# Kernel tuning notes

Measured on AMD Instinct MI355X. Metric: run time of the kernel, lower is better.

## Reference

```python
import jax, jax.numpy as jnp
import numpy as np

NUM_HEADS = 8
DIM = 256
SCALE = (DIM // NUM_HEADS) ** -0.5  # head_dim = dim // nhead = 32


def setup_inputs() -> dict:
    key = jax.random.key(0)
    k1, k2, k3, k4, k5 = jax.random.split(key, 5)
    B, N = 1, 4096
    qk = jax.random.normal(k1, (B, N, 3 * DIM), dtype=jnp.float32)
    v_cls = jax.random.normal(k2, (B, N, 2 * DIM), dtype=jnp.float32)
    masks = jax.random.uniform(k3, (B, N, N), dtype=jnp.float32)
    # torch Linear weights stored as [in, out] for x @ W
    W_qk = jax.random.normal(k4, (3 * DIM, 6 * DIM), dtype=jnp.float32) * (3 * DIM) ** -0.5
    W_v = jax.random.normal(k5, (2 * DIM, 2 * DIM), dtype=jnp.float32) * (2 * DIM) ** -0.5
    return {"qk": qk, "v_cls": v_cls, "masks": masks, "W_qk": W_qk, "W_v": W_v}


def reference(qk, v_cls, masks, W_qk, W_v):
    B, N, C_qk = qk.shape
    C_cls = v_cls.shape[-1]
    H = NUM_HEADS
    hd_qk = C_qk // H   # 96
    hd_v = C_cls // H   # 64

    # qk projection: [B,N,6*dim] -> (2,B,H,N,hd_qk)
    proj = (qk @ W_qk).reshape(B, N, 2, H, hd_qk).transpose(2, 0, 3, 1, 4)
    q, k = proj[0], proj[1]                      # [B,H,N,hd_qk]
    v = (v_cls @ W_v).reshape(B, N, H, hd_v).transpose(0, 2, 1, 3)  # [B,H,N,hd_v]

    attn = jnp.einsum('bhnd,bhmd->bhnm', q, k) * SCALE
    attn = jax.nn.softmax(attn, axis=-1)

    # post-softmax mask-mul and renorm by mask-sum and head count
    m = masks[:, None]                           # [B,1,N,N] broadcast over heads
    attn = attn * m / (H * jnp.sum(m, axis=-1, keepdims=True))
    # attn_drop with p=0.0 is identity in eval

    x_cls = jnp.einsum('bhnm,bhmd->bhnd', attn, v)
    return x_cls.transpose(0, 2, 1, 3).reshape(B, N, C_cls)
```

## Files before the change

### kernel.cpp

```cpp
#include <hip/hip_runtime.h>

typedef __attribute__((ext_vector_type(8))) _Float16 half8;
typedef __attribute__((ext_vector_type(4))) _Float16 half4;
typedef __attribute__((ext_vector_type(2))) _Float16 half2;
typedef __attribute__((ext_vector_type(2))) __fp16 fp16x2;
typedef __attribute__((ext_vector_type(4))) float f32x4;

#define N_SEQ 4096
#define HD_QK 96
#define HD_V  64
#define NHEADS 8
#define QSCALE 0.25505545556f
#define ESHIFT 8.0f

union PKC { fp16x2 p; half2 h; };

__device__ inline half2 pk_cvt(float a, float b) {
    PKC u;
    u.p = __builtin_amdgcn_cvt_pkrtz(a, b);
    return u.h;
}

__device__ inline half8 cvt8(float4 a, float4 b) {
    half8 h;
    h[0] = (_Float16)a.x; h[1] = (_Float16)a.y; h[2] = (_Float16)a.z; h[3] = (_Float16)a.w;
    h[4] = (_Float16)b.x; h[5] = (_Float16)b.y; h[6] = (_Float16)b.z; h[7] = (_Float16)b.w;
    return h;
}

__device__ inline void cast_blk(const float* __restrict__ in, _Float16* __restrict__ out,
                                int blk, int t) {
    size_t i = ((size_t)blk * 256 + t) * 8;
    float4 a = *(const float4*)(in + i);
    float4 b = *(const float4*)(in + i + 4);
    *(half8*)(out + i) = cvt8(a, b);
}

__global__ __launch_bounds__(256) void prep(
    const float* __restrict__ qk, const float* __restrict__ v_cls,
    const float* __restrict__ masks, const float* __restrict__ W_qk,
    const float* __restrict__ W_v,
    _Float16* __restrict__ Xh, _Float16* __restrict__ Vch,
    _Float16* __restrict__ Msw, float* __restrict__ Msum,
    _Float16* __restrict__ Wqkt, _Float16* __restrict__ Wvt)
{
    __shared__ float tile[32][33];
    const int bx = blockIdx.x, t = threadIdx.x;
    if (bx < 1536) {
        cast_blk(qk, Xh, bx, t);
    } else if (bx < 2560) {
        cast_blk(v_cls, Vch, bx - 1536, t);
    } else if (bx < 3968) {
        const bool big = bx < 3712;
        const int id = big ? bx - 2560 : bx - 3712;
        const int nx = big ? 48 : 16;
        const int C = big ? 1536 : 512, R = big ? 768 : 512;
        const float* in = big ? W_qk : W_v;
        _Float16* out = big ? Wqkt : Wvt;
        int cx = id % nx, cy = id / nx;
        int tx = t & 31, ty = t >> 5;
        int c0 = cx * 32, r0 = cy * 32;
        for (int k = 0; k < 4; k++)
            tile[ty + 8 * k][tx] = in[(size_t)(r0 + ty + 8 * k) * C + c0 + tx];
        __syncthreads();
        for (int k = 0; k < 4; k++)
            out[(size_t)(c0 + ty + 8 * k) * R + r0 + tx] = (_Float16)tile[tx][ty + 8 * k];
    } else {
        const int m = bx - 3968;
        const int q = m >> 1;
        const int k0 = (m & 1) * 2048 + t * 8;
        const float* src = masks + (size_t)q * N_SEQ + k0;
        float4 a = *(const float4*)src;
        float4 b = *(const float4*)(src + 4);
        const int q0b = q >> 6, l15 = q & 15, nt = (q >> 4) & 3;
        const int kb = k0 >> 6, wsl = (k0 >> 4) & 3, qd = (k0 >> 2) & 3;
        _Float16* dst = Msw + ((size_t)(q0b * 64 + kb) * 4 + wsl) * 1024
                            + l15 * 64 + qd * 16 + nt * 4;
        half4 h0 = {(_Float16)a.x, (_Float16)a.y, (_Float16)a.z, (_Float16)a.w};
        half4 h1 = {(_Float16)b.x, (_Float16)b.y, (_Float16)b.z, (_Float16)b.w};
        *(half4*)dst = h0;
        *(half4*)(dst + 16) = h1;
        float s = (a.x + a.y) + (a.z + a.w) + (b.x + b.y) + (b.z + b.w);
        for (int off = 1; off < 64; off <<= 1) s += __shfl_xor(s, off);
        if ((t & 63) == 0) atomicAdd(&Msum[q], s);
    }
}

__global__ __launch_bounds__(256) void proj_fused(
    const _Float16* __restrict__ Xh, const _Float16* __restrict__ Vch,
    const _Float16* __restrict__ Wqkt, const _Float16* __restrict__ Wvt,
    _Float16* __restrict__ Qh, _Float16* __restrict__ Kh,
    _Float16* __restrict__ Vtg)
{
    __shared__ _Float16 smem[2 * 128 * 72];
    _Float16 (*Xs)[72] = (_Float16 (*)[72])smem;
    _Float16 (*Ws)[72] = (_Float16 (*)[72])(smem + 128 * 72);

    const int t = threadIdx.x;
    const int lane = t & 63, wv = t >> 6;
    const int quad = lane >> 4, l15 = lane & 15;
    const bool qkmode = blockIdx.x < 12;
    const int n0 = qkmode ? blockIdx.x * 128 : (blockIdx.x - 12) * 128;
    const int row0 = blockIdx.y * 128;
    const int K = qkmode ? 768 : 512;
    const _Float16* X = qkmode ? Xh : Vch;
    const _Float16* Wt = qkmode ? Wqkt : Wvt;

    const int mB = (wv & 1) * 64, nB = (wv >> 1) * 64;
    const int sr = t >> 1, sk = (t & 1) * 32;

    const f32x4 fzero = {0.f, 0.f, 0.f, 0.f};
    f32x4 acc[4][4];
    for (int i = 0; i < 4; i++)
        for (int j = 0; j < 4; j++) acc[i][j] = fzero;

    for (int k0 = 0; k0 < K; k0 += 64) {
        __syncthreads();
        {
            const _Float16* xp = X + (size_t)(row0 + sr) * K + k0 + sk;
            *(half8*)&Xs[sr][sk]      = *(const half8*)xp;
            *(half8*)&Xs[sr][sk + 8]  = *(const half8*)(xp + 8);
            *(half8*)&Xs[sr][sk + 16] = *(const half8*)(xp + 16);
            *(half8*)&Xs[sr][sk + 24] = *(const half8*)(xp + 24);
            const _Float16* wp = Wt + (size_t)(n0 + sr) * K + k0 + sk;
            *(half8*)&Ws[sr][sk]      = *(const half8*)wp;
            *(half8*)&Ws[sr][sk + 8]  = *(const half8*)(wp + 8);
            *(half8*)&Ws[sr][sk + 16] = *(const half8*)(wp + 16);
            *(half8*)&Ws[sr][sk + 24] = *(const half8*)(wp + 24);
        }
        __syncthreads();
        for (int c = 0; c < 2; c++) {
            half8 af[4], bf[4];
            for (int i = 0; i < 4; i++)
                af[i] = *(const half8*)&Xs[mB + 16 * i + l15][c * 32 + quad * 8];
            for (int j = 0; j < 4; j++)
                bf[j] = *(const half8*)&Ws[nB + 16 * j + l15][c * 32 + quad * 8];
            for (int i = 0; i < 4; i++)
                for (int j = 0; j < 4; j++)
                    acc[i][j] = __builtin_amdgcn_mfma_f32_16x16x32_f16(af[i], bf[j], acc[i][j], 0, 0, 0);
        }
    }

    __syncthreads();
    _Float16 (*Ct)[136] = (_Float16 (*)[136])smem;
    for (int j = 0; j < 4; j++) {
        int col = n0 + nB + 16 * j + l15;
        float scl = (qkmode && col < 768) ? QSCALE : 1.0f;
        for (int i = 0; i < 4; i++)
            for (int r = 0; r < 4; r++)
                Ct[mB + 16 * i + quad * 4 + r][nB + 16 * j + l15] =
                    (_Float16)(acc[i][j][r] * scl);
    }
    __syncthreads();

    if (qkmode) {
        for (int e = 0; e < 8; e++) {
            int id = e * 256 + t;
            int row = id >> 4, cc = id & 15;
            int col = n0 + cc * 8;
            int w = col >= 768 ? 1 : 0;
            int rem = col - w * 768;
            int h = rem / 96, d = rem - h * 96;
            _Float16* dst = w ? Kh : Qh;
            *(half8*)&dst[((size_t)h * N_SEQ + row0 + row) * HD_QK + d] =
                *(const half8*)&Ct[row][cc * 8];
        }
    } else {
        for (int e = 0; e < 4; e++) {
            int id = e * 256 + t;
            int col = id >> 3, rc = id & 7;
            int c = n0 + col;
            int h = c >> 6, d = c & 63;
            half8 v0, v1;
            for (int k = 0; k < 8; k++) {
                v0[k] = Ct[rc * 16 + k][col];
                v1[k] = Ct[rc * 16 + 8 + k][col];
            }
            _Float16* dst = &Vtg[((size_t)h * HD_V + d) * N_SEQ + row0 + rc * 16];
            *(half8*)dst = v0;
            *(half8*)(dst + 8) = v1;
        }
    }
}

__global__ __launch_bounds__(256, 3) void flash_attn(
    const _Float16* __restrict__ Qh, const _Float16* __restrict__ Kh,
    const _Float16* __restrict__ Vtg, const _Float16* __restrict__ Msw,
    _Float16* __restrict__ Owsh, float* __restrict__ Lws)
{
    __shared__ __align__(16) float Ob[2][64][68];
    __shared__ float Lb[2][64];

    const int t = threadIdx.x;
    const int lane = t & 63, w = t >> 6;
    const int quad = lane >> 4, l15 = lane & 15;
    const int bx = blockIdx.x;
    const int q0b = bx & 63;
    const int hz = bx >> 6;
    const int head = hz & 7;
    const int z = hz >> 3;
    const int q0 = q0b * 64;
    const int kb0 = 21 * z, kbE = (z == 2) ? 64 : kb0 + 21;

    half8 qf[3][4];
    for (int nt = 0; nt < 4; nt++) {
        const _Float16* qp = Qh + ((size_t)head * N_SEQ + q0 + 16 * nt + l15) * HD_QK + 8 * quad;
        for (int c = 0; c < 3; c++)
            qf[c][nt] = *(const half8*)(qp + 32 * c);
    }

    const _Float16* kbase = Kh + ((size_t)head * N_SEQ + 16 * w + l15) * HD_QK + 8 * quad;
    const _Float16* vbase = Vtg + ((size_t)head * HD_V + l15) * N_SEQ + 16 * w + 4 * quad;
    const _Float16* mbase = Msw + ((size_t)(q0b * 64 + kb0) * 4 + w) * 1024
                                + (l15 * 4 + quad) * 16;

    const f32x4 fzero = {0.f, 0.f, 0.f, 0.f};
    f32x4 oacc[4][4];
    for (int nt = 0; nt < 4; nt++)
        for (int v = 0; v < 4; v++) oacc[nt][v] = fzero;
    float lsum[4] = {0.f, 0.f, 0.f, 0.f};

    half8 kf[3];
    half4 vf[4];
    half8 m01, m23;
    {
        const _Float16* kp = kbase + (size_t)kb0 * 64 * HD_QK;
        for (int c = 0; c < 3; c++) kf[c] = *(const half8*)(kp + 32 * c);
        const _Float16* vp = vbase + kb0 * 64;
        for (int v = 0; v < 4; v++) vf[v] = *(const half4*)(vp + (size_t)(16 * v) * N_SEQ);
        m01 = *(const half8*)mbase;
        m23 = *(const half8*)(mbase + 8);
    }

    for (int kb = kb0; kb < kbE; kb++) {
        const int kn = (kb + 1 < kbE) ? kb + 1 : kb;

        f32x4 sT[4];
        for (int nt = 0; nt < 4; nt++) sT[nt] = fzero;
        for (int c = 0; c < 3; c++)
            for (int nt = 0; nt < 4; nt++)
                sT[nt] = __builtin_amdgcn_mfma_f32_16x16x32_f16(kf[c], qf[c][nt], sT[nt], 0, 0, 0);
        {
            const _Float16* kp = kbase + (size_t)kn * 64 * HD_QK;
            for (int c = 0; c < 3; c++) kf[c] = *(const half8*)(kp + 32 * c);
        }

        half4 af[4];
        {
            half2 mh[8];
            for (int i = 0; i < 4; i++) {
                mh[i]     = half2{m01[2 * i], m01[2 * i + 1]};
                mh[4 + i] = half2{m23[2 * i], m23[2 * i + 1]};
            }
            for (int nt = 0; nt < 4; nt++) {
                float p0 = exp2f(sT[nt][0] - ESHIFT);
                float p1 = exp2f(sT[nt][1] - ESHIFT);
                float p2 = exp2f(sT[nt][2] - ESHIFT);
                float p3 = exp2f(sT[nt][3] - ESHIFT);
                lsum[nt] += (p0 + p1) + (p2 + p3);
                half2 lo = pk_cvt(p0, p1) * mh[2 * nt];
                half2 hi = pk_cvt(p2, p3) * mh[2 * nt + 1];
                af[nt] = half4{lo[0], lo[1], hi[0], hi[1]};
            }
        }
        {
            const _Float16* mp = mbase + (size_t)(kn - kb0) * 4096;
            m01 = *(const half8*)mp;
            m23 = *(const half8*)(mp + 8);
        }

        for (int nt = 0; nt < 4; nt++)
            for (int v = 0; v < 4; v++)
                oacc[nt][v] = __builtin_amdgcn_mfma_f32_16x16x16f16(af[nt], vf[v], oacc[nt][v], 0, 0, 0);
        {
            const _Float16* vp = vbase + kn * 64;
            for (int v = 0; v < 4; v++) vf[v] = *(const half4*)(vp + (size_t)(16 * v) * N_SEQ);
        }
    }

    for (int nt = 0; nt < 4; nt++) {
        lsum[nt] += __shfl_xor(lsum[nt], 16);
        lsum[nt] += __shfl_xor(lsum[nt], 32);
    }

    if (w & 1) {
        for (int nt = 0; nt < 4; nt++) {
            for (int v = 0; v < 4; v++)
                for (int r = 0; r < 4; r++)
                    Ob[w >> 1][16 * nt + 4 * quad + r][16 * v + l15] = oacc[nt][v][r];
            if (quad == 0) Lb[w >> 1][16 * nt + l15] = lsum[nt];
        }
    }
    __syncthreads();
    if (!(w & 1)) {
        for (int nt = 0; nt < 4; nt++) {
            for (int v = 0; v < 4; v++)
                for (int r = 0; r < 4; r++)
                    Ob[w >> 1][16 * nt + 4 * quad + r][16 * v + l15] += oacc[nt][v][r];
            if (quad == 0) Lb[w >> 1][16 * nt + l15] += lsum[nt];
        }
    }
    __syncthreads();

    {
        int row = t >> 2, c0 = (t & 3) * 16;
        _Float16* obase = Owsh + (size_t)z * N_SEQ * 512 + (size_t)(q0 + row) * 512
                          + head * HD_V + c0;
        for (int g = 0; g < 2; g++) {
            half8 h;
            for (int j = 0; j < 8; j++)
                h[j] = (_Float16)(Ob[0][row][c0 + 8 * g + j] + Ob[1][row][c0 + 8 * g + j]);
            *(half8*)(obase + 8 * g) = h;
        }
        if (t < 64)
            Lws[((size_t)z * NHEADS + head) * N_SEQ + q0 + t] = Lb[0][t] + Lb[1][t];
    }
}

__global__ __launch_bounds__(256) void finalize(
    const _Float16* __restrict__ Owsh, const float* __restrict__ Lws,
    const float* __restrict__ Msum, float* __restrict__ out)
{
    const size_t ZSTR = (size_t)N_SEQ * 512;
    size_t o = ((size_t)blockIdx.x * 256 + threadIdx.x) * 8;
    int q = (int)(o >> 9);
    int head = (int)((o & 511) >> 6);
    half8 p0 = *(const half8*)(Owsh + o);
    half8 p1 = *(const half8*)(Owsh + ZSTR + o);
    half8 p2 = *(const half8*)(Owsh + 2 * ZSTR + o);
    float l = Lws[(size_t)head * N_SEQ + q]
            + Lws[((size_t)NHEADS + head) * N_SEQ + q]
            + Lws[((size_t)2 * NHEADS + head) * N_SEQ + q];
    float inv = 1.0f / (l * (float)NHEADS * Msum[q]);
    float4 r0, r1;
    r0.x = ((float)p0[0] + (float)p1[0] + (float)p2[0]) * inv;
    r0.y = ((float)p0[1] + (float)p1[1] + (float)p2[1]) * inv;
    r0.z = ((float)p0[2] + (float)p1[2] + (float)p2[2]) * inv;
    r0.w = ((float)p0[3] + (float)p1[3] + (float)p2[3]) * inv;
    r1.x = ((float)p0[4] + (float)p1[4] + (float)p2[4]) * inv;
    r1.y = ((float)p0[5] + (float)p1[5] + (float)p2[5]) * inv;
    r1.z = ((float)p0[6] + (float)p1[6] + (float)p2[6]) * inv;
    r1.w = ((float)p0[7] + (float)p1[7] + (float)p2[7]) * inv;
    *(float4*)(out + o) = r0;
    *(float4*)(out + o + 4) = r1;
}

extern "C" void kernel_launch(void* const* d_in, const int* in_sizes, int n_in,
                              void* d_out, int out_size, void* d_ws, size_t ws_size,
                              hipStream_t stream) {
    const float* qk    = (const float*)d_in[0];
    const float* v_cls = (const float*)d_in[1];
    const float* masks = (const float*)d_in[2];
    const float* W_qk  = (const float*)d_in[3];
    const float* W_v   = (const float*)d_in[4];
    float* out = (float*)d_out;

    char* wsp = (char*)d_ws;
    _Float16* Xh   = (_Float16*)(wsp);
    _Float16* Vch  = (_Float16*)(wsp + (size_t)6291456);
    _Float16* Wqkt = (_Float16*)(wsp + (size_t)10485760);
    _Float16* Wvt  = (_Float16*)(wsp + (size_t)12845056);
    _Float16* Owsh = (_Float16*)(wsp);
    size_t off = 13631488;
    auto allocB = [&](size_t bytes) { char* p = wsp + off; off += (bytes + 255) & ~(size_t)255; return p; };
    _Float16* Qh   = (_Float16*)allocB((size_t)NHEADS * N_SEQ * HD_QK * 2);
    _Float16* Kh   = (_Float16*)allocB((size_t)NHEADS * N_SEQ * HD_QK * 2);
    _Float16* Vtg  = (_Float16*)allocB((size_t)NHEADS * HD_V * N_SEQ * 2);
    _Float16* Msw  = (_Float16*)allocB((size_t)N_SEQ * N_SEQ * 2);
    float*    Msum = (float*)allocB((size_t)N_SEQ * 4);
    float*    Lws  = (float*)allocB((size_t)3 * NHEADS * N_SEQ * 4);
    (void)ws_size;

    dim3 blk(256);
    (void)hipMemsetAsync(Msum, 0, N_SEQ * sizeof(float), stream);
    prep<<<dim3(12160), blk, 0, stream>>>(
        qk, v_cls, masks, W_qk, W_v, Xh, Vch, Msw, Msum, Wqkt, Wvt);

    proj_fused<<<dim3(16, N_SEQ / 128), blk, 0, stream>>>(
        Xh, Vch, Wqkt, Wvt, Qh, Kh, Vtg);

    flash_attn<<<dim3(1536), blk, 0, stream>>>(
        Qh, Kh, Vtg, Msw, Owsh, Lws);

    finalize<<<dim3((N_SEQ * 512) / (256 * 8)), blk, 0, stream>>>(
        Owsh, Lws, Msum, out);
}
```

Measured before the change: 281.5 us.

## Stage K/V tiles through LDS with async global_load_lds double buffering

Per-wave K and V tiles are now fetched with global_load_lds directly into a double-buffered shared-memory region, replacing register-prefetched global loads. A waitcnt at the top of each iteration lets the next tile's fetch overlap the current MFMA and exp work. The softmax shift is folded into the MFMA accumulator init, which removes one subtraction per score. The cost is more LDS per block, which may hurt occupancy, and vmcnt-based ordering that depends on the mask loads also being counted correctly.

```diff
diff --git a/kernel.cpp b/kernel.cpp
--- a/kernel.cpp
+++ b/kernel.cpp
@@ -34,6 +34,12 @@
     float4 a = *(const float4*)(in + i);
     float4 b = *(const float4*)(in + i + 4);
     *(half8*)(out + i) = cvt8(a, b);
+}
+
+__device__ __forceinline__ void gl16(const void* g, void* l) {
+    __builtin_amdgcn_global_load_lds(
+        (const __attribute__((address_space(1))) unsigned int*)g,
+        (__attribute__((address_space(3))) unsigned int*)l, 16, 0, 0);
 }
 
 __global__ __launch_bounds__(256) void prep(
@@ -188,8 +194,7 @@
     const _Float16* __restrict__ Vtg, const _Float16* __restrict__ Msw,
     _Float16* __restrict__ Owsh, float* __restrict__ Lws)
 {
-    __shared__ __align__(16) float Ob[2][64][68];
-    __shared__ float Lb[2][64];
+    __shared__ __align__(16) char smem[41472];
 
     const int t = threadIdx.x;
     const int lane = t & 63, w = t >> 6;
@@ -209,40 +214,74 @@
             qf[c][nt] = *(const half8*)(qp + 32 * c);
     }
 
-    const _Float16* kbase = Kh + ((size_t)head * N_SEQ + 16 * w + l15) * HD_QK + 8 * quad;
-    const _Float16* vbase = Vtg + ((size_t)head * HD_V + l15) * N_SEQ + 16 * w + 4 * quad;
+    const char* kgb = (const char*)Kh
+        + ((size_t)(head * N_SEQ + 16 * w + l15) * HD_QK + 8 * quad) * 2;
+    const char* vgb = (const char*)Vtg
+        + ((size_t)(head * HD_V + lane) * N_SEQ) * 2 + 32 * w;
     const _Float16* mbase = Msw + ((size_t)(q0b * 64 + kb0) * 4 + w) * 1024
                                 + (l15 * 4 + quad) * 16;
 
+    char* stW = smem + w * 10240;
+
     const f32x4 fzero = {0.f, 0.f, 0.f, 0.f};
+    const f32x4 minit = {-ESHIFT, -ESHIFT, -ESHIFT, -ESHIFT};
     f32x4 oacc[4][4];
     for (int nt = 0; nt < 4; nt++)
         for (int v = 0; v < 4; v++) oacc[nt][v] = fzero;
     float lsum[4] = {0.f, 0.f, 0.f, 0.f};
 
-    half8 kf[3];
-    half4 vf[4];
     half8 m01, m23;
+
     {
-        const _Float16* kp = kbase + (size_t)kb0 * 64 * HD_QK;
-        for (int c = 0; c < 3; c++) kf[c] = *(const half8*)(kp + 32 * c);
-        const _Float16* vp = vbase + kb0 * 64;
-        for (int v = 0; v < 4; v++) vf[v] = *(const half4*)(vp + (size_t)(16 * v) * N_SEQ);
-        m01 = *(const half8*)mbase;
-        m23 = *(const half8*)(mbase + 8);
-    }
-
-    for (int kb = kb0; kb < kbE; kb++) {
-        const int kn = (kb + 1 < kbE) ? kb + 1 : kb;
+        char* kd = stW;
+        const char* ks = kgb + (size_t)kb0 * 12288;
+        gl16(ks, kd);
+        gl16(ks + 64, kd + 1024);
+        gl16(ks + 128, kd + 2048);
+        char* vd = stW + 3072;
+        const char* vs = vgb + (size_t)kb0 * 128;
+        gl16(vs, vd);
+        gl16(vs + 16, vd + 1024);
+    }
+    m01 = *(const half8*)mbase;
+    m23 = *(const half8*)(mbase + 8);
+
+    int cur = 0;
+    for (int j = kb0; j < kbE; j++, cur ^= 1) {
+        asm volatile("s_waitcnt vmcnt(2)" ::: "memory");
+        __builtin_amdgcn_sched_barrier(0);
+
+        const char* kl = stW + cur * 5120;
+        half8 kf[3];
+        kf[0] = *(const half8*)(kl + lane * 16);
+        kf[1] = *(const half8*)(kl + 1024 + lane * 16);
+        kf[2] = *(const half8*)(kl + 2048 + lane * 16);
+        const char* vl = kl + 3072 + (quad >> 1) * 1024 + l15 * 16 + (quad & 1) * 8;
+        half4 vf[4];
+        vf[0] = *(const half4*)(vl);
+        vf[1] = *(const half4*)(vl + 256);
+        vf[2] = *(const half4*)(vl + 512);
+        vf[3] = *(const half4*)(vl + 768);
+
+        const int jn = (j + 1 < kbE) ? j + 1 : j;
+        {
+            char* kd = stW + (cur ^ 1) * 5120;
+            const char* ks = kgb + (size_t)jn * 12288;
+            gl16(ks, kd);
+            gl16(ks + 64, kd + 1024);
+            gl16(ks + 128, kd + 2048);
+            char* vd = kd + 3072;
+            const char* vs = vgb + (size_t)jn * 128;
+            gl16(vs, vd);
+            gl16(vs + 16, vd + 1024);
+        }
 
         f32x4 sT[4];
-        for (int nt = 0; nt < 4; nt++) sT[nt] = fzero;
-        for (int c = 0; c < 3; c++)
-            for (int nt = 0; nt < 4; nt++)
-                sT[nt] = __builtin_amdgcn_mfma_f32_16x16x32_f16(kf[c], qf[c][nt], sT[nt], 0, 0, 0);
-        {
-            const _Float16* kp = kbase + (size_t)kn * 64 * HD_QK;
-            for (int c = 0; c < 3; c++) kf[c] = *(const half8*)(kp + 32 * c);
+        for (int nt = 0; nt < 4; nt++) {
+            f32x4 s = __builtin_amdgcn_mfma_f32_16x16x32_f16(kf[0], qf[0][nt], minit, 0, 0, 0);
+            s = __builtin_amdgcn_mfma_f32_16x16x32_f16(kf[1], qf[1][nt], s, 0, 0, 0);
+            s = __builtin_amdgcn_mfma_f32_16x16x32_f16(kf[2], qf[2][nt], s, 0, 0, 0);
+            sT[nt] = s;
         }
 
         half4 af[4];
@@ -253,10 +292,10 @@
                 mh[4 + i] = half2{m23[2 * i], m23[2 * i + 1]};
             }
             for (int nt = 0; nt < 4; nt++) {
-                float p0 = exp2f(sT[nt][0] - ESHIFT);
-                float p1 = exp2f(sT[nt][1] - ESHIFT);
-                float p2 = exp2f(sT[nt][2] - ESHIFT);
-                float p3 = exp2f(sT[nt][3] - ESHIFT);
+                float p0 = exp2f(sT[nt][0]);
+                float p1 = exp2f(sT[nt][1]);
+                float p2 = exp2f(sT[nt][2]);
+                float p3 = exp2f(sT[nt][3]);
                 lsum[nt] += (p0 + p1) + (p2 + p3);
                 half2 lo = pk_cvt(p0, p1) * mh[2 * nt];
                 half2 hi = pk_cvt(p2, p3) * mh[2 * nt + 1];
@@ -264,7 +303,7 @@
             }
         }
         {
-            const _Float16* mp = mbase + (size_t)(kn - kb0) * 4096;
+            const _Float16* mp = mbase + (size_t)(jn - kb0) * 4096;
             m01 = *(const half8*)mp;
             m23 = *(const half8*)(mp + 8);
         }
@@ -272,11 +311,12 @@
         for (int nt = 0; nt < 4; nt++)
             for (int v = 0; v < 4; v++)
                 oacc[nt][v] = __builtin_amdgcn_mfma_f32_16x16x16f16(af[nt], vf[v], oacc[nt][v], 0, 0, 0);
-        {
-            const _Float16* vp = vbase + kn * 64;
-            for (int v = 0; v < 4; v++) vf[v] = *(const half4*)(vp + (size_t)(16 * v) * N_SEQ);
-        }
-    }
+    }
+
+    __syncthreads();
+
+    float (*Ob)[64][68] = (float (*)[64][68])smem;
+    float (*Lb)[64] = (float (*)[64])(smem + 34816);
 
     for (int nt = 0; nt < 4; nt++) {
         lsum[nt] += __shfl_xor(lsum[nt], 16);
@@ -308,8 +348,8 @@
                           + head * HD_V + c0;
         for (int g = 0; g < 2; g++) {
             half8 h;
-            for (int j = 0; j < 8; j++)
-                h[j] = (_Float16)(Ob[0][row][c0 + 8 * g + j] + Ob[1][row][c0 + 8 * g + j]);
+            for (int j2 = 0; j2 < 8; j2++)
+                h[j2] = (_Float16)(Ob[0][row][c0 + 8 * g + j2] + Ob[1][row][c0 + 8 * g + j2]);
             *(half8*)(obase + 8 * g) = h;
         }
         if (t < 64)
```

New measurement: 274.7 us. 2.4% less time.
